# Kernel optimization log

Measured on AMD Instinct MI355X. Metric: run time of the kernel, lower is better.

The kernel has to match this reference:

```python
import jax, jax.numpy as jnp
import numpy as np

L, H, S, D = 32, 8, 1024, 128   # stacked kv: total_layers x [1,H,S,D]
V = 128000                        # vocab
BEAM = 3
HIST = 16


def setup_inputs() -> dict:
    key = jax.random.key(0)
    k1, k2, k3 = jax.random.split(key, 3)
    return {
        "kv": jax.random.normal(k1, (L, 1, H, S, D), dtype=jnp.float32),
        "logits": jax.random.normal(k2, (1, V), dtype=jnp.float32),
        "save_id": jax.random.randint(k3, (BEAM, HIST), 0, V, dtype=jnp.int32),
        "repeat_penality": jnp.ones((BEAM, V), dtype=jnp.float32),
        "penality_value": jnp.full((1,), 0.9, dtype=jnp.float32),
        "beam_size": BEAM,
    }


def reference(kv, logits, save_id, repeat_penality, penality_value, beam_size):
    # log_softmax + sorted top-k over vocab
    logp = jax.nn.log_softmax(logits, axis=-1)                 # [1, V]
    top_prob, top_idx = jax.lax.top_k(logp, beam_size)         # [1, beam] (sorted desc)

    # repeat every layer's KV cache beam_size times along its leading dim
    # kv: [L, 1, H, S, D] -> [L, beam, H, S, D]
    kv_rep = jnp.tile(kv, (1, beam_size, 1, 1, 1))

    top_idx_t = jnp.transpose(top_idx, (0, 1)).T               # [beam, 1]
    # gather-multiply-scatter repetition penalty (indices unique per row)
    rows = jnp.arange(beam_size)[:, None]                      # [beam, 1]
    repeat_penality = repeat_penality.at[rows, top_idx_t].multiply(penality_value[0])

    top_idx_i = top_idx_t.astype(jnp.int32)                    # [beam, 1]
    save_id = jnp.concatenate([save_id, top_idx_i], axis=-1)   # [beam, HIST+1]
    max_logits_idx = top_idx_i[0]                              # [1]

    return (kv_rep, top_idx_i, save_id, repeat_penality, top_prob.T, max_logits_idx)
```

## Files before the change

kernel.cpp:

```cpp
#include <hip/hip_runtime.h>
#include <math.h>

#define V      128000
#define BEAM   3
#define HIST   16
#define NPART  125

#define O_KV   0
#define O_IDX  100663296
#define O_SAVE (O_IDX + BEAM)
#define O_RP   (O_SAVE + BEAM*(HIST+1))
#define O_PROB (O_RP + BEAM*V)
#define O_MAX  (O_PROB + BEAM)

__device__ __forceinline__ void ins3(float v, int idx,
    float& v0, int& i0, float& v1, int& i1, float& v2, int& i2) {
  if (v > v0)      { v2=v1; i2=i1; v1=v0; i1=i0; v0=v; i0=idx; }
  else if (v > v1) { v2=v1; i2=i1; v1=v;  i1=idx; }
  else if (v > v2) { v2=v;  i2=idx; }
}

__global__ __launch_bounds__(256) void topk_partial(const float* __restrict__ logits,
                                                    float* __restrict__ part) {
  const int gid  = blockIdx.x * 256 + threadIdx.x;
  const float4 x4 = ((const float4*)logits)[gid];
  const int base = gid << 2;

  float m = -INFINITY, s = 0.f;
  float v0 = -INFINITY, v1 = -INFINITY, v2 = -INFINITY;
  int   i0 = 0, i1 = 0, i2 = 0;

  float xs[4] = {x4.x, x4.y, x4.z, x4.w};
#pragma unroll
  for (int j = 0; j < 4; ++j) {
    const float x  = xs[j];
    const float nm = fmaxf(m, x);
    s = s * __expf(m - nm) + __expf(x - nm);
    m = nm;
    ins3(x, base + j, v0, i0, v1, i1, v2, i2);
  }

  const int lane = threadIdx.x & 63;
#pragma unroll
  for (int d = 32; d >= 1; d >>= 1) {
    float om  = __shfl_down(m,  d, 64);
    float os  = __shfl_down(s,  d, 64);
    float ov0 = __shfl_down(v0, d, 64); int oi0 = __shfl_down(i0, d, 64);
    float ov1 = __shfl_down(v1, d, 64); int oi1 = __shfl_down(i1, d, 64);
    float ov2 = __shfl_down(v2, d, 64); int oi2 = __shfl_down(i2, d, 64);
    if (lane + d < 64) {
      const float nm = fmaxf(m, om);
      s = s * __expf(m - nm) + os * __expf(om - nm);
      m = nm;
      ins3(ov0, oi0, v0, i0, v1, i1, v2, i2);
      ins3(ov1, oi1, v0, i0, v1, i1, v2, i2);
      ins3(ov2, oi2, v0, i0, v1, i1, v2, i2);
    }
  }

  __shared__ float sm[4][8];
  const int wave = threadIdx.x >> 6;
  if (lane == 0) {
    sm[wave][0] = m;  sm[wave][1] = s;
    sm[wave][2] = v0; sm[wave][3] = v1; sm[wave][4] = v2;
    sm[wave][5] = __int_as_float(i0);
    sm[wave][6] = __int_as_float(i1);
    sm[wave][7] = __int_as_float(i2);
  }
  __syncthreads();
  if (threadIdx.x == 0) {
#pragma unroll
    for (int w = 1; w < 4; ++w) {
      const float om = sm[w][0], os = sm[w][1];
      const float nm = fmaxf(m, om);
      s = s * __expf(m - nm) + os * __expf(om - nm);
      m = nm;
      ins3(sm[w][2], __float_as_int(sm[w][5]), v0, i0, v1, i1, v2, i2);
      ins3(sm[w][3], __float_as_int(sm[w][6]), v0, i0, v1, i1, v2, i2);
      ins3(sm[w][4], __float_as_int(sm[w][7]), v0, i0, v1, i1, v2, i2);
    }
    float* p = part + blockIdx.x * 8;
    p[0] = m;  p[1] = s;
    p[2] = v0; p[3] = v1; p[4] = v2;
    p[5] = __int_as_float(i0);
    p[6] = __int_as_float(i1);
    p[7] = __int_as_float(i2);
  }
}

__global__ __launch_bounds__(64) void topk_final(const float* __restrict__ part,
                                                 const int* __restrict__ save_id,
                                                 float* __restrict__ out,
                                                 int* __restrict__ ws_idx) {
  const int t = threadIdx.x;
  float m = -INFINITY, s = 0.f;
  float v0 = -INFINITY, v1 = -INFINITY, v2 = -INFINITY;
  int   i0 = 0, i1 = 0, i2 = 0;

  {
    const float* p = part + t * 8;
    m = p[0]; s = p[1];
    v0 = p[2]; v1 = p[3]; v2 = p[4];
    i0 = __float_as_int(p[5]); i1 = __float_as_int(p[6]); i2 = __float_as_int(p[7]);
  }
  if (t + 64 < NPART) {
    const float* p = part + (t + 64) * 8;
    const float om = p[0], os = p[1];
    const float nm = fmaxf(m, om);
    s = s * __expf(m - nm) + os * __expf(om - nm);
    m = nm;
    ins3(p[2], __float_as_int(p[5]), v0, i0, v1, i1, v2, i2);
    ins3(p[3], __float_as_int(p[6]), v0, i0, v1, i1, v2, i2);
    ins3(p[4], __float_as_int(p[7]), v0, i0, v1, i1, v2, i2);
  }

#pragma unroll
  for (int d = 32; d >= 1; d >>= 1) {
    float om  = __shfl_down(m,  d, 64);
    float os  = __shfl_down(s,  d, 64);
    float ov0 = __shfl_down(v0, d, 64); int oi0 = __shfl_down(i0, d, 64);
    float ov1 = __shfl_down(v1, d, 64); int oi1 = __shfl_down(i1, d, 64);
    float ov2 = __shfl_down(v2, d, 64); int oi2 = __shfl_down(i2, d, 64);
    if (t + d < 64) {
      const float nm = fmaxf(m, om);
      s = s * __expf(m - nm) + os * __expf(om - nm);
      m = nm;
      ins3(ov0, oi0, v0, i0, v1, i1, v2, i2);
      ins3(ov1, oi1, v0, i0, v1, i1, v2, i2);
      ins3(ov2, oi2, v0, i0, v1, i1, v2, i2);
    }
  }

  __shared__ float res[BEAM];
  if (t == 0) {
    const float logZ = m + logf(s);
    out[O_IDX + 0] = (float)i0;
    out[O_IDX + 1] = (float)i1;
    out[O_IDX + 2] = (float)i2;
    out[O_PROB + 0] = v0 - logZ;
    out[O_PROB + 1] = v1 - logZ;
    out[O_PROB + 2] = v2 - logZ;
    out[O_MAX] = (float)i0;
    ws_idx[0] = i0; ws_idx[1] = i1; ws_idx[2] = i2;
    res[0] = (float)i0; res[1] = (float)i1; res[2] = (float)i2;
  }
  __syncthreads();
  if (t < BEAM * (HIST + 1)) {
    const int b = t / (HIST + 1);
    const int j = t - b * (HIST + 1);
    out[O_SAVE + t] = (j < HIST) ? (float)save_id[b * HIST + j] : res[b];
  }
}

#define KV_BLOCKS 32768
#define RP_BLOCKS 375

__global__ __launch_bounds__(256) void kv_penalty(const float4* __restrict__ kv,
                                                  const float* __restrict__ rp,
                                                  const float* __restrict__ penv,
                                                  const int* __restrict__ ws_idx,
                                                  float4* __restrict__ kv_out,
                                                  float* __restrict__ rp_out) {
  const int b = blockIdx.x;
  if (b < KV_BLOCKS) {
    const int i     = (b << 8) | threadIdx.x;
    const int chunk = i >> 18;
    const int off   = i & 262143;
    const float4 v  = kv[i];
    const int dbase = (chunk * 3) << 18;
    kv_out[dbase + off]              = v;
    kv_out[dbase + (1 << 18) + off]  = v;
    kv_out[dbase + (2 << 18) + off]  = v;
  } else {
    const int i   = ((b - KV_BLOCKS) << 8) | threadIdx.x;
    const int row = i / 32000;
    const int off = i - row * 32000;
    float4 v = ((const float4*)(rp + row * V))[off];
    const int tgt = ws_idx[row];
    const int vb  = off << 2;
    if (tgt >= vb && tgt < vb + 4) {
      const float p = penv[0];
      float* vf = (float*)&v;
      vf[tgt - vb] *= p;
    }
    float2* d = (float2*)(rp_out + row * V) + off * 2;
    d[0] = make_float2(v.x, v.y);
    d[1] = make_float2(v.z, v.w);
  }
}

extern "C" void kernel_launch(void* const* d_in, const int* in_sizes, int n_in,
                              void* d_out, int out_size, void* d_ws, size_t ws_size,
                              hipStream_t stream) {
  const float* kv      = (const float*)d_in[0];
  const float* logits  = (const float*)d_in[1];
  const int*   save_id = (const int*)d_in[2];
  const float* rp      = (const float*)d_in[3];
  const float* penv    = (const float*)d_in[4];
  float* out = (float*)d_out;

  float* part  = (float*)d_ws;
  int* ws_idx  = (int*)d_ws + 2048;

  topk_partial<<<NPART, 256, 0, stream>>>(logits, part);
  topk_final<<<1, 64, 0, stream>>>(part, save_id, out, ws_idx);
  kv_penalty<<<KV_BLOCKS + RP_BLOCKS, 256, 0, stream>>>(
      (const float4*)kv, rp, penv, ws_idx, (float4*)(out + O_KV), out + O_RP);
}
```

Before: 511.0 us.

## Fuse top-k into single block and batch KV tile copy with nontemporal ops

Replaces the two-kernel top-k reduction (partial plus final) with one 1024-thread block that loops over the vocabulary, removing one launch and the workspace round-trip. The KV tiling copy now has each thread load four float4 values and store each three times using nontemporal loads and stores, with four times fewer blocks. Penalty blocks are moved to the front of the grid. The single-block top-k serialises the logits scan onto one CU, which may lengthen the critical path before the dependent kernel.

```diff
diff --git a/kernel.cpp b/kernel.cpp
--- a/kernel.cpp
+++ b/kernel.cpp
@@ -4,7 +4,6 @@
 #define V      128000
 #define BEAM   3
 #define HIST   16
-#define NPART  125
 
 #define O_KV   0
 #define O_IDX  100663296
@@ -13,6 +12,8 @@
 #define O_PROB (O_RP + BEAM*V)
 #define O_MAX  (O_PROB + BEAM)
 
+typedef float f4 __attribute__((ext_vector_type(4)));
+
 __device__ __forceinline__ void ins3(float v, int idx,
     float& v0, int& i0, float& v1, int& i1, float& v2, int& i2) {
   if (v > v0)      { v2=v1; i2=i1; v1=v0; i1=i0; v0=v; i0=idx; }
@@ -20,27 +21,29 @@
   else if (v > v2) { v2=v;  i2=idx; }
 }
 
-__global__ __launch_bounds__(256) void topk_partial(const float* __restrict__ logits,
-                                                    float* __restrict__ part) {
-  const int gid  = blockIdx.x * 256 + threadIdx.x;
-  const float4 x4 = ((const float4*)logits)[gid];
-  const int base = gid << 2;
-
+__global__ __launch_bounds__(1024) void topk_kernel(const float* __restrict__ logits,
+                                                    const int* __restrict__ save_id,
+                                                    float* __restrict__ out,
+                                                    int* __restrict__ ws_idx) {
+  const int t = threadIdx.x;
   float m = -INFINITY, s = 0.f;
   float v0 = -INFINITY, v1 = -INFINITY, v2 = -INFINITY;
   int   i0 = 0, i1 = 0, i2 = 0;
 
-  float xs[4] = {x4.x, x4.y, x4.z, x4.w};
+  for (int k = t; k < 32000; k += 1024) {
+    const f4 x4 = ((const f4*)logits)[k];
+    const int base = k << 2;
 #pragma unroll
-  for (int j = 0; j < 4; ++j) {
-    const float x  = xs[j];
-    const float nm = fmaxf(m, x);
-    s = s * __expf(m - nm) + __expf(x - nm);
-    m = nm;
-    ins3(x, base + j, v0, i0, v1, i1, v2, i2);
+    for (int j = 0; j < 4; ++j) {
+      const float x  = x4[j];
+      const float nm = fmaxf(m, x);
+      s = s * __expf(m - nm) + __expf(x - nm);
+      m = nm;
+      ins3(x, base + j, v0, i0, v1, i1, v2, i2);
+    }
   }
 
-  const int lane = threadIdx.x & 63;
+  const int lane = t & 63;
 #pragma unroll
   for (int d = 32; d >= 1; d >>= 1) {
     float om  = __shfl_down(m,  d, 64);
@@ -58,8 +61,9 @@
     }
   }
 
-  __shared__ float sm[4][8];
-  const int wave = threadIdx.x >> 6;
+  __shared__ float sm[16][8];
+  __shared__ float res[BEAM];
+  const int wave = t >> 6;
   if (lane == 0) {
     sm[wave][0] = m;  sm[wave][1] = s;
     sm[wave][2] = v0; sm[wave][3] = v1; sm[wave][4] = v2;
@@ -68,9 +72,9 @@
     sm[wave][7] = __int_as_float(i2);
   }
   __syncthreads();
-  if (threadIdx.x == 0) {
+  if (t == 0) {
 #pragma unroll
-    for (int w = 1; w < 4; ++w) {
+    for (int w = 1; w < 16; ++w) {
       const float om = sm[w][0], os = sm[w][1];
       const float nm = fmaxf(m, om);
       s = s * __expf(m - nm) + os * __expf(om - nm);
@@ -79,60 +83,6 @@
       ins3(sm[w][3], __float_as_int(sm[w][6]), v0, i0, v1, i1, v2, i2);
       ins3(sm[w][4], __float_as_int(sm[w][7]), v0, i0, v1, i1, v2, i2);
     }
-    float* p = part + blockIdx.x * 8;
-    p[0] = m;  p[1] = s;
-    p[2] = v0; p[3] = v1; p[4] = v2;
-    p[5] = __int_as_float(i0);
-    p[6] = __int_as_float(i1);
-    p[7] = __int_as_float(i2);
-  }
-}
-
-__global__ __launch_bounds__(64) void topk_final(const float* __restrict__ part,
-                                                 const int* __restrict__ save_id,
-                                                 float* __restrict__ out,
-                                                 int* __restrict__ ws_idx) {
-  const int t = threadIdx.x;
-  float m = -INFINITY, s = 0.f;
-  float v0 = -INFINITY, v1 = -INFINITY, v2 = -INFINITY;
-  int   i0 = 0, i1 = 0, i2 = 0;
-
-  {
-    const float* p = part + t * 8;
-    m = p[0]; s = p[1];
-    v0 = p[2]; v1 = p[3]; v2 = p[4];
-    i0 = __float_as_int(p[5]); i1 = __float_as_int(p[6]); i2 = __float_as_int(p[7]);
-  }
-  if (t + 64 < NPART) {
-    const float* p = part + (t + 64) * 8;
-    const float om = p[0], os = p[1];
-    const float nm = fmaxf(m, om);
-    s = s * __expf(m - nm) + os * __expf(om - nm);
-    m = nm;
-    ins3(p[2], __float_as_int(p[5]), v0, i0, v1, i1, v2, i2);
-    ins3(p[3], __float_as_int(p[6]), v0, i0, v1, i1, v2, i2);
-    ins3(p[4], __float_as_int(p[7]), v0, i0, v1, i1, v2, i2);
-  }
-
-#pragma unroll
-  for (int d = 32; d >= 1; d >>= 1) {
-    float om  = __shfl_down(m,  d, 64);
-    float os  = __shfl_down(s,  d, 64);
-    float ov0 = __shfl_down(v0, d, 64); int oi0 = __shfl_down(i0, d, 64);
-    float ov1 = __shfl_down(v1, d, 64); int oi1 = __shfl_down(i1, d, 64);
-    float ov2 = __shfl_down(v2, d, 64); int oi2 = __shfl_down(i2, d, 64);
-    if (t + d < 64) {
-      const float nm = fmaxf(m, om);
-      s = s * __expf(m - nm) + os * __expf(om - nm);
-      m = nm;
-      ins3(ov0, oi0, v0, i0, v1, i1, v2, i2);
-      ins3(ov1, oi1, v0, i0, v1, i1, v2, i2);
-      ins3(ov2, oi2, v0, i0, v1, i1, v2, i2);
-    }
-  }
-
-  __shared__ float res[BEAM];
-  if (t == 0) {
     const float logZ = m + logf(s);
     out[O_IDX + 0] = (float)i0;
     out[O_IDX + 1] = (float)i1;
@@ -152,40 +102,49 @@
   }
 }
 
-#define KV_BLOCKS 32768
 #define RP_BLOCKS 375
+#define KV_BLOCKS 8192
 
-__global__ __launch_bounds__(256) void kv_penalty(const float4* __restrict__ kv,
+__global__ __launch_bounds__(256) void kv_penalty(const f4* __restrict__ kv,
                                                   const float* __restrict__ rp,
                                                   const float* __restrict__ penv,
                                                   const int* __restrict__ ws_idx,
-                                                  float4* __restrict__ kv_out,
+                                                  f4* __restrict__ kv_out,
                                                   float* __restrict__ rp_out) {
   const int b = blockIdx.x;
-  if (b < KV_BLOCKS) {
-    const int i     = (b << 8) | threadIdx.x;
-    const int chunk = i >> 18;
-    const int off   = i & 262143;
-    const float4 v  = kv[i];
-    const int dbase = (chunk * 3) << 18;
-    kv_out[dbase + off]              = v;
-    kv_out[dbase + (1 << 18) + off]  = v;
-    kv_out[dbase + (2 << 18) + off]  = v;
+  if (b >= RP_BLOCKS) {
+    const int kb    = b - RP_BLOCKS;
+    const int chunk = kb >> 8;
+    const int off0  = ((kb & 255) << 10) + threadIdx.x;
+    const f4* __restrict__ src = kv + ((long)chunk << 18);
+    f4* __restrict__ dst = kv_out + ((long)(chunk * 3) << 18);
+
+    f4 a0 = __builtin_nontemporal_load(src + off0);
+    f4 a1 = __builtin_nontemporal_load(src + off0 + 256);
+    f4 a2 = __builtin_nontemporal_load(src + off0 + 512);
+    f4 a3 = __builtin_nontemporal_load(src + off0 + 768);
+
+#pragma unroll
+    for (int r = 0; r < 3; ++r) {
+      f4* d = dst + ((long)r << 18);
+      __builtin_nontemporal_store(a0, d + off0);
+      __builtin_nontemporal_store(a1, d + off0 + 256);
+      __builtin_nontemporal_store(a2, d + off0 + 512);
+      __builtin_nontemporal_store(a3, d + off0 + 768);
+    }
   } else {
-    const int i   = ((b - KV_BLOCKS) << 8) | threadIdx.x;
+    const int i   = (b << 8) | threadIdx.x;
     const int row = i / 32000;
     const int off = i - row * 32000;
-    float4 v = ((const float4*)(rp + row * V))[off];
+    f4 v = ((const f4*)(rp + row * V))[off];
     const int tgt = ws_idx[row];
     const int vb  = off << 2;
     if (tgt >= vb && tgt < vb + 4) {
-      const float p = penv[0];
-      float* vf = (float*)&v;
-      vf[tgt - vb] *= p;
+      v[tgt - vb] *= penv[0];
     }
     float2* d = (float2*)(rp_out + row * V) + off * 2;
-    d[0] = make_float2(v.x, v.y);
-    d[1] = make_float2(v.z, v.w);
+    d[0] = make_float2(v[0], v[1]);
+    d[1] = make_float2(v[2], v[3]);
   }
 }
 
@@ -198,12 +157,9 @@
   const float* rp      = (const float*)d_in[3];
   const float* penv    = (const float*)d_in[4];
   float* out = (float*)d_out;
+  int* ws_idx = (int*)d_ws;
 
-  float* part  = (float*)d_ws;
-  int* ws_idx  = (int*)d_ws + 2048;
-
-  topk_partial<<<NPART, 256, 0, stream>>>(logits, part);
-  topk_final<<<1, 64, 0, stream>>>(part, save_id, out, ws_idx);
-  kv_penalty<<<KV_BLOCKS + RP_BLOCKS, 256, 0, stream>>>(
-      (const float4*)kv, rp, penv, ws_idx, (float4*)(out + O_KV), out + O_RP);
+  topk_kernel<<<1, 1024, 0, stream>>>(logits, save_id, out, ws_idx);
+  kv_penalty<<<RP_BLOCKS + KV_BLOCKS, 256, 0, stream>>>(
+      (const f4*)kv, rp, penv, ws_idx, (f4*)(out + O_KV), out + O_RP);
 }
```

Measured after the change: 670.2 us. +31.2%, slower.
